# Kernel optimization log

Hardware: AMD Instinct MI355X
Metric: run time of the kernel (lower is better)

## Reference

```python
import jax, jax.numpy as jnp
import numpy as np

# q_config constants
W_IN, E_IN = 8, 4          # data_in_width, data_in_exponent_width
R_W = 6                     # data_r_width
W_OUT, E_OUT = 8, 4        # data_out_width, data_out_exponent_width (= data_n_width)
EXP_SUM_UF = 4              # exp_sum_underflow_bits
DIV_UF = 4                  # division_underflow_bits
W_DATA, E_DATA = 8, 4      # data_width, data_exponent_width

N, D = 8192, 2048


def integer_quantizer(x, width, frac_width):
    s = 2.0 ** frac_width
    lo, hi = -(2.0 ** (width - 1)), 2.0 ** (width - 1) - 1
    return jnp.clip(jnp.round(x * s), lo, hi) / s


def integer_floor_quantizer(x, width, frac_width):
    s = 2.0 ** frac_width
    lo, hi = -(2.0 ** (width - 1)), 2.0 ** (width - 1) - 1
    return jnp.clip(jnp.floor(x * s), lo, hi) / s


def mxint_quant(x, width, exponent_width):
    # MXInt block quantization with parallelism [1,1]: per-element shared exponent.
    e_hi, e_lo = 2.0 ** (exponent_width - 1) - 1, -(2.0 ** (exponent_width - 1))
    ax = jnp.abs(x)
    e = jnp.ceil(jnp.log2(jnp.where(ax == 0, 1.0, ax)))
    e = jnp.clip(e, e_lo, e_hi)
    scale = 2.0 ** (width - 1)
    m = jnp.clip(jnp.round(x * 2.0 ** (-e) * scale), -scale, scale - 1)
    qx = m * 2.0 ** e / scale
    return qx, m, e


def setup_inputs() -> dict:
    key = jax.random.key(0)
    x = jax.random.normal(key, (N, D), dtype=jnp.float32)
    return {"x": x}


def reference(x):
    # ---- MXIntHardwareExp: quantize input, range-reduce x = r + n*ln2 ----
    qx, _, _ = mxint_quant(x, W_IN, E_IN)
    log2e, _, _ = mxint_quant(jnp.float32(np.log2(np.e)), 8, 4)
    y = qx * log2e
    y = integer_floor_quantizer(y, E_OUT + R_W - 1, R_W - 1)
    n = jnp.floor(y)
    r = y - n                                # r in [0, 1)
    mexp = integer_quantizer(2.0 ** r, W_OUT, W_OUT - 2) * 2.0 ** (W_OUT - 2)
    eexp = n                                 # qexp = mexp * 2^eexp / 2^(W_OUT-2)

    # ---- exp_sum: exponent-aligned integer accumulation over dim 1 ----
    ms = (mexp * 2.0 ** EXP_SUM_UF).T        # [D, N]
    es = eexp.T                              # [D, N]

    def step(carry, me):
        out, emax = carry
        mi, ei = me
        new_emax = jnp.maximum(emax, ei)
        out = jnp.floor(out * 2.0 ** (emax - new_emax)) + jnp.floor(mi * 2.0 ** (ei - new_emax))
        return (out, new_emax), None

    (mexp_sum, eexp_sum), _ = jax.lax.scan(step, (ms[0], es[0]), (ms[1:], es[1:]))
    # mexp_sum, eexp_sum: [N]

    # ---- division: per-element mantissa integer division by the sum ----
    mout = jnp.floor(mexp * 2.0 ** (DIV_UF + EXP_SUM_UF) / mexp_sum[:, None])
    eout = eexp - eexp_sum[:, None]
    qout = mout * 2.0 ** eout / 2.0 ** DIV_UF
    qout, _, _ = mxint_quant(qout, W_DATA, E_DATA)
    return qout
```

## Files before the change

kernel.cpp:

```cpp
#include <hip/hip_runtime.h>


#define D_DIM 2048
#define TPB   256
#define RPB   4

__device__ __constant__ int c_mexp_tab[32] = {
    64, 65, 67, 68, 70, 71, 73, 74, 76, 78, 79, 81, 83, 85, 87, 89,
    91, 92, 95, 97, 99, 101, 103, 105, 108, 110, 112, 115, 117, 120, 123, 125
};

__global__ __launch_bounds__(TPB) void mxint_softmax_kernel(const float* __restrict__ x,
                                                            float* __restrict__ out) {
    const int t    = threadIdx.x;
    const int lane = t & 63;
    const int wid  = t >> 6;
    const int row  = blockIdx.x * RPB + wid;

    __shared__ float s_res[RPB][512];
    float* wt = s_res[wid];

#pragma unroll
    for (int q = 0; q < 8; ++q) {
        const int      idx   = q * 64 + lane;
        const unsigned mout  = (unsigned)(idx & 31);
        const int      eoutn = idx >> 5;
        const int      bl    = 32 - __clz((int)(mout | 1u));
        const int      pw2   = ((mout & (mout - 1u)) == 0u) ? 1 : 0;
        const int      clog  = bl - pw2;
        const int      s     = min(7 - clog, 11 - eoutn);
        const int      rs    = 8 - s;
        const unsigned u     = mout << 8;
        const unsigned bse   = u >> rs;
        const unsigned frac  = u & ((1u << rs) - 1u);
        const unsigned half  = 1u << (rs - 1);
        unsigned m2 = bse + (((frac > half) || (frac == half && (bse & 1u))) ? 1u : 0u);
        m2 = min(m2, 127u);
        const int ef = max(clog - eoutn - 4, -8);
        wt[idx] = (float)m2 * __uint_as_float((unsigned)(ef + 120) << 23);
    }

    const int tv = c_mexp_tab[lane & 31];

    const float* xr = x + (size_t)row * D_DIM;
    float4 v[8];
#pragma unroll
    for (int i = 0; i < 8; ++i)
        v[i] = *(const float4*)(xr + i * 256 + lane * 4);

    unsigned pk[16];
    unsigned partial = 0;
    int carry8 = 0;

#pragma unroll
    for (int i = 0; i < 8; ++i) {
        const float xs4[4] = {v[i].x, v[i].y, v[i].z, v[i].w};
        int me[4], e8[4], a[4];
#pragma unroll
        for (int k = 0; k < 4; ++k) {
            const float    xv   = xs4[k];
            const unsigned bits = __float_as_uint(xv) & 0x7fffffffu;
            const int      eb   = (int)((bits + 0x7fffffu) >> 23);
            const int      ebc  = min(134, max(119, eb));
            const float    su   = __uint_as_float((unsigned)(261 - ebc) << 23);
            int mi = (int)rintf(xv * su);
            mi = min(127, max(-128, mi));
            int yq = (mi * 46) >> (134 - ebc);
            yq = min(255, max(-256, yq));
            e8[k] = (yq >> 5) + 8;
            me[k] = __builtin_amdgcn_ds_bpermute((yq & 31) << 2, tv);
            a[k]  = (k == 0) ? e8[0] : max(a[k - 1], e8[k]);
        }

        int sc = a[3];
#pragma unroll
        for (int d = 1; d < 64; d <<= 1) {
            const int o = __shfl_up(sc, d, 64);
            if (lane >= d) sc = max(sc, o);
        }
        int ex = __shfl_up(sc, 1, 64);
        if (lane == 0) ex = 0;
        const int base = max(carry8, ex);

#pragma unroll
        for (int k = 0; k < 4; ++k) {
            const int E8 = max(base, a[k]);
            const unsigned c = ((unsigned)me[k] << 4) >> (E8 - e8[k]);
            partial += c << E8;
        }
        pk[2 * i]     = (unsigned)me[0] | ((unsigned)e8[0] << 8)
                      | ((unsigned)me[1] << 16) | ((unsigned)e8[1] << 24);
        pk[2 * i + 1] = (unsigned)me[2] | ((unsigned)e8[2] << 8)
                      | ((unsigned)me[3] << 16) | ((unsigned)e8[3] << 24);

        carry8 = max(carry8, __shfl(sc, 63, 64));
    }

    unsigned long long p64 = partial;
#pragma unroll
    for (int d = 32; d >= 1; d >>= 1) p64 += __shfl_xor(p64, d, 64);

    const int      Estar8 = carry8;
    const unsigned msum   = (unsigned)(p64 >> Estar8);
    const unsigned magic  = (unsigned)(274877906944.0 / (double)msum) + 1u;

    float* orow = out + (size_t)row * D_DIM;
#pragma unroll
    for (int i = 0; i < 8; ++i) {
        float r4[4];
#pragma unroll
        for (int k = 0; k < 4; ++k) {
            const unsigned p   = pk[2 * i + (k >> 1)];
            const unsigned sh  = (unsigned)(k & 1) * 16u;
            const unsigned mel = (p >> sh) & 0xffu;
            const unsigned ee8 = (p >> (sh + 8)) & 0xffu;
            const unsigned mout  = __umulhi(mel << 8, magic) >> 6;
            const int      eoutn = Estar8 - (int)ee8;
            r4[k] = wt[(eoutn << 5) | (int)mout];
        }
        const float4 o4 = {r4[0], r4[1], r4[2], r4[3]};
        *(float4*)(orow + i * 256 + lane * 4) = o4;
    }
}

extern "C" void kernel_launch(void* const* d_in, const int* in_sizes, int n_in,
                              void* d_out, int out_size, void* d_ws, size_t ws_size,
                              hipStream_t stream) {
    const float* x = (const float*)d_in[0];
    float*       o = (float*)d_out;
    const int rows = in_sizes[0] / D_DIM;
    mxint_softmax_kernel<<<rows / RPB, TPB, 0, stream>>>(x, o);
}
```

Baseline: 114.1 us.

## Batch wave prefix-max scans with packed byte max and compute mexp via exp2

Replaces the eight sequential per-chunk wave prefix-max scans with a single scan over packed per-chunk maxima, four bytes per register, using a SWAR byte-wise max. Computes the 2^r mantissa with the hardware exp2 plus rounding instead of a ds_bpermute table lookup, hoists the global loads above the shared-table setup, and narrows the first reduction step to 32 bits. This cuts cross-lane shuffle traffic and latency in the serial accumulation. The risks are exp2 rounding mismatches against the table and extra register and ALU pressure from repacking.

```diff
diff --git a/kernel.cpp b/kernel.cpp
--- a/kernel.cpp
+++ b/kernel.cpp
@@ -5,10 +5,12 @@
 #define TPB   256
 #define RPB   4
 
-__device__ __constant__ int c_mexp_tab[32] = {
-    64, 65, 67, 68, 70, 71, 73, 74, 76, 78, 79, 81, 83, 85, 87, 89,
-    91, 92, 95, 97, 99, 101, 103, 105, 108, 110, 112, 115, 117, 120, 123, 125
-};
+__device__ __forceinline__ unsigned bmax4(unsigned x, unsigned y) {
+    const unsigned d     = (x | 0x80808080u) - y;
+    const unsigned flags = d & 0x80808080u;
+    const unsigned mask  = (flags - (flags >> 7)) | flags;
+    return (x & mask) | (y & ~mask);
+}
 
 __global__ __launch_bounds__(TPB) void mxint_softmax_kernel(const float* __restrict__ x,
                                                             float* __restrict__ out) {
@@ -17,9 +19,14 @@
     const int wid  = t >> 6;
     const int row  = blockIdx.x * RPB + wid;
 
+    const float* xr = x + (size_t)row * D_DIM;
+    float4 v[8];
+#pragma unroll
+    for (int i = 0; i < 8; ++i)
+        v[i] = *(const float4*)(xr + i * 256 + lane * 4);
+
     __shared__ float s_res[RPB][512];
     float* wt = s_res[wid];
-
 #pragma unroll
     for (int q = 0; q < 8; ++q) {
         const int      idx   = q * 64 + lane;
@@ -40,22 +47,13 @@
         wt[idx] = (float)m2 * __uint_as_float((unsigned)(ef + 120) << 23);
     }
 
-    const int tv = c_mexp_tab[lane & 31];
-
-    const float* xr = x + (size_t)row * D_DIM;
-    float4 v[8];
-#pragma unroll
-    for (int i = 0; i < 8; ++i)
-        v[i] = *(const float4*)(xr + i * 256 + lane * 4);
-
     unsigned pk[16];
-    unsigned partial = 0;
-    int carry8 = 0;
-
+    unsigned pe0 = 0, pe1 = 0;
 #pragma unroll
     for (int i = 0; i < 8; ++i) {
         const float xs4[4] = {v[i].x, v[i].y, v[i].z, v[i].w};
-        int me[4], e8[4], a[4];
+        int me[4], e8[4];
+        int rmax = 0;
 #pragma unroll
         for (int k = 0; k < 4; ++k) {
             const float    xv   = xs4[k];
@@ -68,39 +66,58 @@
             int yq = (mi * 46) >> (134 - ebc);
             yq = min(255, max(-256, yq));
             e8[k] = (yq >> 5) + 8;
-            me[k] = __builtin_amdgcn_ds_bpermute((yq & 31) << 2, tv);
-            a[k]  = (k == 0) ? e8[0] : max(a[k - 1], e8[k]);
+            const float a = fmaf((float)(yq & 31), 0.03125f, 6.0f);
+            me[k] = (int)rintf(__builtin_amdgcn_exp2f(a));
+            rmax  = max(rmax, e8[k]);
         }
-
-        int sc = a[3];
-#pragma unroll
-        for (int d = 1; d < 64; d <<= 1) {
-            const int o = __shfl_up(sc, d, 64);
-            if (lane >= d) sc = max(sc, o);
-        }
-        int ex = __shfl_up(sc, 1, 64);
-        if (lane == 0) ex = 0;
-        const int base = max(carry8, ex);
-
-#pragma unroll
-        for (int k = 0; k < 4; ++k) {
-            const int E8 = max(base, a[k]);
-            const unsigned c = ((unsigned)me[k] << 4) >> (E8 - e8[k]);
-            partial += c << E8;
-        }
+        if (i < 4) pe0 |= (unsigned)rmax << (i * 8);
+        else       pe1 |= (unsigned)rmax << ((i - 4) * 8);
         pk[2 * i]     = (unsigned)me[0] | ((unsigned)e8[0] << 8)
                       | ((unsigned)me[1] << 16) | ((unsigned)e8[1] << 24);
         pk[2 * i + 1] = (unsigned)me[2] | ((unsigned)e8[2] << 8)
                       | ((unsigned)me[3] << 16) | ((unsigned)e8[3] << 24);
-
-        carry8 = max(carry8, __shfl(sc, 63, 64));
     }
 
-    unsigned long long p64 = partial;
+    unsigned s0 = pe0, s1 = pe1;
 #pragma unroll
-    for (int d = 32; d >= 1; d >>= 1) p64 += __shfl_xor(p64, d, 64);
+    for (int d = 1; d < 64; d <<= 1) {
+        const unsigned o0 = __shfl_up(s0, d, 64);
+        const unsigned o1 = __shfl_up(s1, d, 64);
+        if (lane >= d) { s0 = bmax4(s0, o0); s1 = bmax4(s1, o1); }
+    }
+    unsigned ex0 = __shfl_up(s0, 1, 64), ex1 = __shfl_up(s1, 1, 64);
+    if (lane == 0) { ex0 = 0; ex1 = 0; }
+    const unsigned bc0 = __shfl(s0, 63, 64), bc1 = __shfl(s1, 63, 64);
 
-    const int      Estar8 = carry8;
+    unsigned partial = 0;
+    int crun = 0;
+#pragma unroll
+    for (int i = 0; i < 8; ++i) {
+        const unsigned exw = (i < 4) ? ex0 : ex1;
+        const unsigned bcw = (i < 4) ? bc0 : bc1;
+        const int      sh8 = (i & 3) * 8;
+        const int      sx  = (int)((exw >> sh8) & 0xffu);
+        const int base = max(crun, sx);
+        int ar = 0;
+#pragma unroll
+        for (int k = 0; k < 4; ++k) {
+            const unsigned p  = pk[2 * i + (k >> 1)];
+            const unsigned ss = (unsigned)(k & 1) * 16u;
+            const int      mev = (int)((p >> ss) & 0xffu);
+            const int      e8v = (int)((p >> (ss + 8)) & 0xffu);
+            ar = max(ar, e8v);
+            const int E8 = max(base, ar);
+            partial += (((unsigned)mev << 4) >> (E8 - e8v)) << E8;
+        }
+        crun = max(crun, (int)((bcw >> sh8) & 0xffu));
+    }
+
+    const unsigned ps = partial + __shfl_xor(partial, 1, 64);
+    unsigned long long p64 = ps;
+#pragma unroll
+    for (int d = 2; d < 64; d <<= 1) p64 += __shfl_xor(p64, d, 64);
+
+    const int      Estar8 = crun;
     const unsigned msum   = (unsigned)(p64 >> Estar8);
     const unsigned magic  = (unsigned)(274877906944.0 / (double)msum) + 1u;
 
@@ -111,9 +128,9 @@
 #pragma unroll
         for (int k = 0; k < 4; ++k) {
             const unsigned p   = pk[2 * i + (k >> 1)];
-            const unsigned sh  = (unsigned)(k & 1) * 16u;
-            const unsigned mel = (p >> sh) & 0xffu;
-            const unsigned ee8 = (p >> (sh + 8)) & 0xffu;
+            const unsigned ss  = (unsigned)(k & 1) * 16u;
+            const unsigned mel = (p >> ss) & 0xffu;
+            const unsigned ee8 = (p >> (ss + 8)) & 0xffu;
             const unsigned mout  = __umulhi(mel << 8, magic) >> 6;
             const int      eoutn = Estar8 - (int)ee8;
             r4[k] = wt[(eoutn << 5) | (int)mout];
```

New measurement: 113.7 us. Within noise of the previous version (-0.3%).

## Split each row across two waves and use a per-row output lookup table

Applied to the files above, without the earlier changes.

Each row is now handled by two wavefronts, each covering half the row, instead of one wave per row. The separate per-chunk shuffle scans become a single scan over packed byte maxima (a byte-wise max trick), and the two halves combine through shared memory. Outputs come from a 512-entry table indexed by the quantized y value, built once per row after the sum is known, so per-element division and quantization are gone. The cost is extra __syncthreads, shared-memory traffic, and twice as many blocks, in exchange for less register pressure and more parallelism per row.

```diff
diff --git a/kernel.cpp b/kernel.cpp
--- a/kernel.cpp
+++ b/kernel.cpp
@@ -3,123 +3,143 @@
 
 #define D_DIM 2048
 #define TPB   256
-#define RPB   4
 
-__device__ __constant__ int c_mexp_tab[32] = {
-    64, 65, 67, 68, 70, 71, 73, 74, 76, 78, 79, 81, 83, 85, 87, 89,
-    91, 92, 95, 97, 99, 101, 103, 105, 108, 110, 112, 115, 117, 120, 123, 125
-};
+__device__ __forceinline__ unsigned bmax4(unsigned x, unsigned y) {
+    const unsigned d     = (x | 0x80808080u) - y;
+    const unsigned flags = d & 0x80808080u;
+    const unsigned mask  = (flags - (flags >> 7)) | flags;
+    return (x & mask) | (y & ~mask);
+}
 
-__global__ __launch_bounds__(TPB) void mxint_softmax_kernel(const float* __restrict__ x,
-                                                            float* __restrict__ out) {
+__global__ __launch_bounds__(TPB, 6) void mxint_softmax_kernel(const float* __restrict__ x,
+                                                               float* __restrict__ out) {
     const int t    = threadIdx.x;
     const int lane = t & 63;
     const int wid  = t >> 6;
-    const int row  = blockIdx.x * RPB + wid;
+    const int half = wid & 1;
+    const int r    = wid >> 1;
+    const int row  = blockIdx.x * 2 + r;
 
-    __shared__ float s_res[RPB][512];
-    float* wt = s_res[wid];
+    __shared__ unsigned short     s_pk[512];
+    __shared__ float              s_fin[2][512];
+    __shared__ int                s_rmax[4];
+    __shared__ unsigned long long s_part[4];
+
+    const size_t base = (size_t)row * D_DIM + half * 1024 + lane * 4;
+    float4 v[4];
+#pragma unroll
+    for (int i = 0; i < 4; ++i)
+        v[i] = *(const float4*)(x + base + i * 256);
 
 #pragma unroll
-    for (int q = 0; q < 8; ++q) {
-        const int      idx   = q * 64 + lane;
-        const unsigned mout  = (unsigned)(idx & 31);
-        const int      eoutn = idx >> 5;
-        const int      bl    = 32 - __clz((int)(mout | 1u));
-        const int      pw2   = ((mout & (mout - 1u)) == 0u) ? 1 : 0;
-        const int      clog  = bl - pw2;
-        const int      s     = min(7 - clog, 11 - eoutn);
-        const int      rs    = 8 - s;
-        const unsigned u     = mout << 8;
-        const unsigned bse   = u >> rs;
-        const unsigned frac  = u & ((1u << rs) - 1u);
-        const unsigned half  = 1u << (rs - 1);
-        unsigned m2 = bse + (((frac > half) || (frac == half && (bse & 1u))) ? 1u : 0u);
+    for (int q = 0; q < 2; ++q) {
+        const int idx = t + 256 * q;
+        const float a = fmaf((float)(idx & 31), 0.03125f, 6.0f);
+        const int  me = (int)rintf(__builtin_amdgcn_exp2f(a));
+        s_pk[idx] = (unsigned short)(me << 4);
+    }
+
+    int yq[16];
+    unsigned pe = 0;
+#pragma unroll
+    for (int i = 0; i < 4; ++i) {
+        const float xs4[4] = {v[i].x, v[i].y, v[i].z, v[i].w};
+        int rmaxr = -256;
+#pragma unroll
+        for (int k = 0; k < 4; ++k) {
+            const unsigned b  = __float_as_uint(xs4[k]) & 0x7fffffffu;
+            const unsigned tb = b + 0x7fffffu;
+            const unsigned tc = min(max(tb, 0x3B800000u), 0x43000000u);
+            const unsigned es = tc & 0xFF800000u;
+            const float    su  = __uint_as_float(0x82800000u - es);
+            const float    fac = __uint_as_float(es + 0xFF380000u);
+            const float    mi  = __builtin_amdgcn_fmed3f(rintf(xs4[k] * su), -128.0f, 127.0f);
+            int y = (int)floorf(mi * fac);
+            y = min(255, max(-256, y));
+            yq[4 * i + k] = y;
+            rmaxr = max(rmaxr, y);
+        }
+        pe |= (unsigned)((rmaxr >> 5) + 8) << (8 * i);
+    }
+
+    unsigned s = pe;
+#pragma unroll
+    for (int d = 1; d < 64; d <<= 1) {
+        const unsigned o = __shfl_up(s, d, 64);
+        if (lane >= d) s = bmax4(s, o);
+    }
+    unsigned ex = __shfl_up(s, 1, 64);
+    if (lane == 0) ex = 0;
+    const unsigned bc = __shfl(s, 63, 64);
+    const int wtot = max(max((int)(bc & 255u), (int)((bc >> 8) & 255u)),
+                         max((int)((bc >> 16) & 255u), (int)(bc >> 24)));
+    s_rmax[wid] = wtot;
+    __syncthreads();
+
+    const int c0 = half ? s_rmax[wid - 1] : 0;
+
+    unsigned partial = 0;
+    int crun = c0;
+#pragma unroll
+    for (int i = 0; i < 4; ++i) {
+        const int sx   = (int)((ex >> (8 * i)) & 255u);
+        int a = max(crun, sx);
+#pragma unroll
+        for (int k = 0; k < 4; ++k) {
+            const int y  = yq[4 * i + k];
+            const int h  = (y >> 5) + 8;
+            a = max(a, h);
+            const unsigned me4 = s_pk[y + 256];
+            partial += (me4 >> (a - h)) << a;
+        }
+        crun = max(crun, (int)((bc >> (8 * i)) & 255u));
+    }
+
+    const unsigned ps = partial + __shfl_xor(partial, 1, 64);
+    unsigned long long p64 = ps;
+#pragma unroll
+    for (int d = 2; d < 64; d <<= 1) p64 += __shfl_xor(p64, d, 64);
+    s_part[wid] = p64;
+    __syncthreads();
+
+    const unsigned long long tot = s_part[2 * r] + s_part[2 * r + 1];
+    const int      Estar8 = max(s_rmax[2 * r], s_rmax[2 * r + 1]);
+    const unsigned msum   = (unsigned)(tot >> Estar8);
+    const unsigned magic  = (unsigned)(274877906944.0 / (double)msum) + 1u;
+
+    const int tr = t & 127;
+#pragma unroll
+    for (int q = 0; q < 4; ++q) {
+        const int      idx  = tr + 128 * q;
+        const unsigned me4  = s_pk[idx];
+        const unsigned mout = __umulhi(me4 << 4, magic) >> 6;
+        const int      e8   = idx >> 5;
+        const int      eoutn = Estar8 - e8;
+        const int      bl   = 32 - __clz((int)(mout | 1u));
+        const int      pw2  = ((mout & (mout - 1u)) == 0u) ? 1 : 0;
+        const int      clog = bl - pw2;
+        const int      sq   = min(7 - clog, 11 - eoutn);
+        const int      rs   = 8 - sq;
+        const unsigned u    = mout << 8;
+        const unsigned bse  = u >> rs;
+        const unsigned frac = u & ((1u << rs) - 1u);
+        const unsigned hlf  = 1u << (rs - 1);
+        unsigned m2 = bse + (((frac > hlf) || (frac == hlf && (bse & 1u))) ? 1u : 0u);
         m2 = min(m2, 127u);
         const int ef = max(clog - eoutn - 4, -8);
-        wt[idx] = (float)m2 * __uint_as_float((unsigned)(ef + 120) << 23);
+        s_fin[r][idx] = (float)m2 * __uint_as_float((unsigned)(ef + 120) << 23);
     }
+    __syncthreads();
 
-    const int tv = c_mexp_tab[lane & 31];
-
-    const float* xr = x + (size_t)row * D_DIM;
-    float4 v[8];
+    float* orow = out + base;
 #pragma unroll
-    for (int i = 0; i < 8; ++i)
-        v[i] = *(const float4*)(xr + i * 256 + lane * 4);
-
-    unsigned pk[16];
-    unsigned partial = 0;
-    int carry8 = 0;
-
-#pragma unroll
-    for (int i = 0; i < 8; ++i) {
-        const float xs4[4] = {v[i].x, v[i].y, v[i].z, v[i].w};
-        int me[4], e8[4], a[4];
-#pragma unroll
-        for (int k = 0; k < 4; ++k) {
-            const float    xv   = xs4[k];
-            const unsigned bits = __float_as_uint(xv) & 0x7fffffffu;
-            const int      eb   = (int)((bits + 0x7fffffu) >> 23);
-            const int      ebc  = min(134, max(119, eb));
-            const float    su   = __uint_as_float((unsigned)(261 - ebc) << 23);
-            int mi = (int)rintf(xv * su);
-            mi = min(127, max(-128, mi));
-            int yq = (mi * 46) >> (134 - ebc);
-            yq = min(255, max(-256, yq));
-            e8[k] = (yq >> 5) + 8;
-            me[k] = __builtin_amdgcn_ds_bpermute((yq & 31) << 2, tv);
-            a[k]  = (k == 0) ? e8[0] : max(a[k - 1], e8[k]);
-        }
-
-        int sc = a[3];
-#pragma unroll
-        for (int d = 1; d < 64; d <<= 1) {
-            const int o = __shfl_up(sc, d, 64);
-            if (lane >= d) sc = max(sc, o);
-        }
-        int ex = __shfl_up(sc, 1, 64);
-        if (lane == 0) ex = 0;
-        const int base = max(carry8, ex);
-
-#pragma unroll
-        for (int k = 0; k < 4; ++k) {
-            const int E8 = max(base, a[k]);
-            const unsigned c = ((unsigned)me[k] << 4) >> (E8 - e8[k]);
-            partial += c << E8;
-        }
-        pk[2 * i]     = (unsigned)me[0] | ((unsigned)e8[0] << 8)
-                      | ((unsigned)me[1] << 16) | ((unsigned)e8[1] << 24);
-        pk[2 * i + 1] = (unsigned)me[2] | ((unsigned)e8[2] << 8)
-                      | ((unsigned)me[3] << 16) | ((unsigned)e8[3] << 24);
-
-        carry8 = max(carry8, __shfl(sc, 63, 64));
-    }
-
-    unsigned long long p64 = partial;
-#pragma unroll
-    for (int d = 32; d >= 1; d >>= 1) p64 += __shfl_xor(p64, d, 64);
-
-    const int      Estar8 = carry8;
-    const unsigned msum   = (unsigned)(p64 >> Estar8);
-    const unsigned magic  = (unsigned)(274877906944.0 / (double)msum) + 1u;
-
-    float* orow = out + (size_t)row * D_DIM;
-#pragma unroll
-    for (int i = 0; i < 8; ++i) {
+    for (int i = 0; i < 4; ++i) {
         float r4[4];
 #pragma unroll
-        for (int k = 0; k < 4; ++k) {
-            const unsigned p   = pk[2 * i + (k >> 1)];
-            const unsigned sh  = (unsigned)(k & 1) * 16u;
-            const unsigned mel = (p >> sh) & 0xffu;
-            const unsigned ee8 = (p >> (sh + 8)) & 0xffu;
-            const unsigned mout  = __umulhi(mel << 8, magic) >> 6;
-            const int      eoutn = Estar8 - (int)ee8;
-            r4[k] = wt[(eoutn << 5) | (int)mout];
-        }
+        for (int k = 0; k < 4; ++k)
+            r4[k] = s_fin[r][yq[4 * i + k] + 256];
         const float4 o4 = {r4[0], r4[1], r4[2], r4[3]};
-        *(float4*)(orow + i * 256 + lane * 4) = o4;
+        *(float4*)(orow + i * 256) = o4;
     }
 }
 
@@ -129,5 +149,5 @@
     const float* x = (const float*)d_in[0];
     float*       o = (float*)d_out;
     const int rows = in_sizes[0] / D_DIM;
-    mxint_softmax_kernel<<<rows / RPB, TPB, 0, stream>>>(x, o);
+    mxint_softmax_kernel<<<rows / 2, TPB, 0, stream>>>(x, o);
 }
```

New measurement: 109.7 us. 1.04x faster.
